# Kernel tuning notes

Measured on AMD Instinct MI355X. Metric: run time of the kernel, lower is better.

Reference implementation:

```python
import jax, jax.numpy as jnp
import numpy as np

MO = 48          # max_output_len (positional slots)
D = 32           # d_inner
NA = 8           # n_actions
STOP = 0
CAT_PRIM, CAT_MOD, CAT_COMB = 0, 1, 2


def _mlp(feats, w1, b1, w2, b2, w3, b3):
    # Linear -> GELU(exact, erf) -> Linear -> GELU -> Linear (torch nn.GELU default is exact)
    h = jax.nn.gelu(feats @ w1.T + b1, approximate=False)
    h = jax.nn.gelu(h @ w2.T + b2, approximate=False)
    return h @ w3.T + b3


def setup_inputs() -> dict:
    key = jax.random.key(0)
    ks = jax.random.split(key, 20)
    B, N = 1024, 16
    inp = {
        'node_cats': jax.random.randint(ks[0], (B, N), 0, 3, dtype=jnp.int32),
        'node_subs': jax.random.randint(ks[1], (B, N), 0, 2, dtype=jnp.int32),
        'node_mask': jax.random.randint(ks[2], (B, N), 0, 2, dtype=jnp.int32),
        'child_left': jax.random.randint(ks[3], (B, N), 0, N, dtype=jnp.int32),
        'child_right': jax.random.randint(ks[4], (B, N), 0, N, dtype=jnp.int32),
        'action_embed': jax.random.normal(ks[5], (NA, D), jnp.float32),
        'mod_w1': jax.random.normal(ks[6], (128, 3), jnp.float32) * 0.1,
        'mod_b1': jax.random.normal(ks[7], (128,), jnp.float32) * 0.02,
        'mod_w2': jax.random.normal(ks[8], (128, 128), jnp.float32) * 0.05,
        'mod_b2': jax.random.normal(ks[9], (128,), jnp.float32) * 0.02,
        'mod_w3': jax.random.normal(ks[10], (MO * MO, 128), jnp.float32) * 0.01,
        'mod_b3': (4.0 * jnp.eye(MO)).flatten(),  # identity-ish init as in torch code
        'comb_w1': jax.random.normal(ks[11], (128, 4), jnp.float32) * 0.1,
        'comb_b1': jax.random.normal(ks[12], (128,), jnp.float32) * 0.02,
        'comb_w2': jax.random.normal(ks[13], (128, 128), jnp.float32) * 0.05,
        'comb_b2': jax.random.normal(ks[14], (128,), jnp.float32) * 0.02,
        'comb_w3': jax.random.normal(ks[15], (MO * 2 * MO, 128), jnp.float32) * 0.01,
        'comb_b3': (4.0 * jnp.eye(MO, 2 * MO)).flatten(),
    }
    return inp


def _forward(node_cats, node_subs, node_mask, child_left, child_right,
             action_embed, mod_w1, mod_b1, mod_w2, mod_b2, mod_w3, mod_b3,
             comb_w1, comb_b1, comb_w2, comb_b2, comb_w3, comb_b3):
    B, N = node_cats.shape
    mask = node_mask.astype(bool)
    cl = jnp.clip(child_left, 0, N - 1)
    cr = jnp.clip(child_right, 0, N - 1)
    prim_mask = (node_cats == CAT_PRIM) & mask
    mod_mask = (node_cats == CAT_MOD) & mask
    comb_mask = (node_cats == CAT_COMB) & mask
    subs01 = jnp.clip(node_subs, 0, 1)
    sub_oh = jax.nn.one_hot(subs01, 2, dtype=jnp.float32)  # (B,N,2)

    # --- primitive init: buffer[0] = action_embed[subs+1], zeros elsewhere ---
    action_ids = jnp.clip(node_subs + 1, 0, NA - 1)
    prim_vecs = action_embed[action_ids]  # (B,N,D)
    buffers = jnp.zeros((B, N, MO, D), jnp.float32)
    buffers = buffers.at[:, :, 0, :].set(prim_vecs * prim_mask[..., None].astype(jnp.float32))
    counts = prim_mask.astype(jnp.float32)  # (B,N)

    # --- modifier stage ---
    child_buf = jnp.take_along_axis(buffers, cl[:, :, None, None], axis=1)  # (B,N,MO,D)
    child_cnt = jnp.take_along_axis(counts, cl, axis=1)  # (B,N)
    feats = jnp.concatenate([child_cnt[..., None] / MO, sub_oh], axis=-1)  # (B,N,3)
    logits = _mlp(feats, mod_w1, mod_b1, mod_w2, mod_b2, mod_w3, mod_b3).reshape(B, N, MO, MO)
    attn = jax.nn.softmax(logits, axis=-1)
    mod_buf = jnp.einsum('bnpq,bnqd->bnpd', attn, child_buf)
    factors = jnp.array([2.0, 3.0], jnp.float32)[subs01]
    mod_cnt = jnp.minimum(child_cnt * factors, float(MO))
    buffers = jnp.where(mod_mask[:, :, None, None], mod_buf, buffers)
    counts = jnp.where(mod_mask, mod_cnt, counts)

    # --- combinator stage ---
    left_buf = jnp.take_along_axis(buffers, cl[:, :, None, None], axis=1)
    right_buf = jnp.take_along_axis(buffers, cr[:, :, None, None], axis=1)
    left_cnt = jnp.take_along_axis(counts, cl, axis=1)
    right_cnt = jnp.take_along_axis(counts, cr, axis=1)
    feats = jnp.concatenate([left_cnt[..., None] / MO, right_cnt[..., None] / MO, sub_oh], axis=-1)  # (B,N,4)
    logits = _mlp(feats, comb_w1, comb_b1, comb_w2, comb_b2, comb_w3, comb_b3).reshape(B, N, MO, 2 * MO)
    attn = jax.nn.softmax(logits, axis=-1)
    concat_buf = jnp.concatenate([left_buf, right_buf], axis=2)  # (B,N,2MO,D)
    comb_buf = jnp.einsum('bnpq,bnqd->bnpd', attn, concat_buf)
    comb_cnt = jnp.minimum(left_cnt + right_cnt, float(MO))
    buffers = jnp.where(comb_mask[:, :, None, None], comb_buf, buffers)
    counts = jnp.where(comb_mask, comb_cnt, counts)

    # --- decode root with tied embedding + stop bias ---
    root_buf = buffers[:, 0, :, :]  # (B,MO,D)
    out = jnp.einsum('bpd,ad->bpa', root_buf, action_embed)  # (B,MO,NA)
    positions = jnp.arange(MO, dtype=jnp.float32)[None, :]  # (1,MO)
    is_stop = (positions >= counts[:, 0:1]).astype(jnp.float32)[..., None]  # (B,MO,1)
    stop_bias = jnp.zeros((NA,), jnp.float32).at[STOP].set(8.0)
    return out + is_stop * stop_bias


def reference(node_cats, node_subs, node_mask, child_left, child_right,
              action_embed, mod_w1, mod_b1, mod_w2, mod_b2, mod_w3, mod_b3,
              comb_w1, comb_b1, comb_w2, comb_b2, comb_w3, comb_b3):
    return _forward(node_cats, node_subs, node_mask, child_left, child_right,
                    action_embed, mod_w1, mod_b1, mod_w2, mod_b2, mod_w3, mod_b3,
                    comb_w1, comb_b1, comb_w2, comb_b2, comb_w3, comb_b3)
```

## Files before the change

kernel.cpp:

```cpp
#include <hip/hip_runtime.h>
#include <hip/hip_bf16.h>
#include <float.h>


#define NNODE 16

#define MODCOL_OFF 0
#define G_OFF      192
#define C0_OFF     256
#define C48_OFF    1792
#define DOTL_OFF   3328
#define DOTR_OFF   6400
#define H2_OFF     9472

__device__ __forceinline__ float gelu_exact(float x) {
    return 0.5f * x * (1.0f + erff(x * 0.70710678118654752f));
}

__device__ __forceinline__ float dot128(const float* __restrict__ w,
                                        const float* __restrict__ h) {
    const float4* w4 = (const float4*)w;
    float s = 0.f;
    #pragma unroll
    for (int i = 0; i < 32; ++i) {
        float4 v = w4[i];
        s += v.x * h[4 * i + 0] + v.y * h[4 * i + 1] +
             v.z * h[4 * i + 2] + v.w * h[4 * i + 3];
    }
    return s;
}

__global__ __launch_bounds__(128) void scan_tables_a(
    const float* __restrict__ E,
    const float* __restrict__ mw1, const float* __restrict__ mb1,
    const float* __restrict__ mw2, const float* __restrict__ mb2,
    const float* __restrict__ mw3, const float* __restrict__ mb3,
    const float* __restrict__ cw1, const float* __restrict__ cb1,
    const float* __restrict__ cw2, const float* __restrict__ cb2,
    float* __restrict__ ws)
{
    __shared__ float h1[128];
    __shared__ float h2s[128];
    __shared__ float lg[48];

    const int tid = threadIdx.x;
    const int blk = blockIdx.x;

    if (blk < 96) {
        const int mm = blk / 48, p = blk % 48;
        const float f0 = 1.0f / 48.0f;
        const float f1 = (mm == 0) ? 1.0f : 0.0f;
        const float f2 = (mm == 1) ? 1.0f : 0.0f;
        h1[tid] = gelu_exact(mw1[tid * 3 + 0] * f0 + mw1[tid * 3 + 1] * f1 +
                             mw1[tid * 3 + 2] * f2 + mb1[tid]);
        __syncthreads();
        h2s[tid] = gelu_exact(dot128(mw2 + tid * 128, h1) + mb2[tid]);
        __syncthreads();
        if (tid < 48)
            lg[tid] = dot128(mw3 + (p * 48 + tid) * 128, h2s) + mb3[p * 48 + tid];
        __syncthreads();
        if (tid < 64) {
            float lv = (tid < 48) ? lg[tid] : -FLT_MAX;
            float mx = lv;
            #pragma unroll
            for (int d = 32; d > 0; d >>= 1) mx = fmaxf(mx, __shfl_xor(mx, d));
            float ev = (tid < 48) ? expf(lv - mx) : 0.f;
            float sm = ev;
            #pragma unroll
            for (int d = 32; d > 0; d >>= 1) sm += __shfl_xor(sm, d);
            if (tid == 0)
                ws[MODCOL_OFF + (2 + mm) * 48 + p] = ev / sm;
        }
        return;
    }
    if (blk == 96) {
        if (tid < 64) {
            const int i = tid >> 3, a = tid & 7;
            float s = 0.f;
            #pragma unroll
            for (int d = 0; d < 32; ++d) s += E[i * 32 + d] * E[a * 32 + d];
            ws[G_OFF + tid] = s;
        }
        return;
    }
    {
        const int c = blk - 97;
        const int csub = c & 1;
        const int rc = (c >> 1) & 3;
        const int lc = (c >> 3) & 3;
        const float f0 = (float)lc / 48.0f;
        const float f1 = (float)rc / 48.0f;
        const float f2 = (csub == 0) ? 1.0f : 0.0f;
        const float f3 = (csub == 1) ? 1.0f : 0.0f;
        h1[tid] = gelu_exact(cw1[tid * 4 + 0] * f0 + cw1[tid * 4 + 1] * f1 +
                             cw1[tid * 4 + 2] * f2 + cw1[tid * 4 + 3] * f3 + cb1[tid]);
        __syncthreads();
        ws[H2_OFF + c * 128 + tid] =
            gelu_exact(dot128(cw2 + tid * 128, h1) + cb2[tid]);
    }
}

__global__ __launch_bounds__(128, 4) void scan_tables_b(
    const float* __restrict__ cw3, const float* __restrict__ cb3,
    float* __restrict__ ws)
{
    __shared__ float h2s[128];
    __shared__ float mc[96];
    __shared__ float lg[96];
    __shared__ float pr[96];
    __shared__ float red[4];

    const int tid = threadIdx.x;
    const int p = blockIdx.x >> 5;
    const int c = blockIdx.x & 31;

    h2s[tid] = ws[H2_OFF + c * 128 + tid];
    if (tid < 96) mc[tid] = ws[MODCOL_OFF + 96 + tid];
    __syncthreads();

    const int j = tid & 3;
    const int rbase = tid >> 2;
    const float4* h24 = (const float4*)h2s;
    #pragma unroll
    for (int o = 0; o < 3; ++o) {
        const int r = o * 32 + rbase;
        const float4* w4 = (const float4*)(cw3 + (p * 96 + r) * 128);
        float s = 0.f;
        #pragma unroll
        for (int i = 0; i < 8; ++i) {
            const int f4i = i * 4 + j;
            float4 w = w4[f4i];
            float4 h = h24[f4i];
            s += w.x * h.x + w.y * h.y + w.z * h.z + w.w * h.w;
        }
        s += __shfl_xor(s, 1);
        s += __shfl_xor(s, 2);
        if (j == 0) lg[r] = s;
    }
    __syncthreads();

    const int wv = tid >> 6;
    float lv = (tid < 96) ? (lg[tid] + cb3[p * 96 + tid]) : -FLT_MAX;
    float m = lv;
    #pragma unroll
    for (int d = 32; d > 0; d >>= 1) m = fmaxf(m, __shfl_xor(m, d));
    if ((tid & 63) == 0) red[wv] = m;
    __syncthreads();
    const float mx = fmaxf(red[0], red[1]);

    float ev = (tid < 96) ? expf(lv - mx) : 0.f;
    if (tid < 96) pr[tid] = ev;
    float sum = ev;
    #pragma unroll
    for (int d = 32; d > 0; d >>= 1) sum += __shfl_xor(sum, d);
    if ((tid & 63) == 0) red[2 + wv] = sum;
    __syncthreads();
    const float inv = 1.0f / (red[2] + red[3]);

    if (tid == 0) {
        ws[C0_OFF + c * 48 + p]  = pr[0]  * inv;
        ws[C48_OFF + c * 48 + p] = pr[48] * inv;
    }
    if (tid < 4) {
        const int mm = tid & 1;
        const int side = tid >> 1;
        const float* q0 = pr + side * 48;
        const float* mr = mc + mm * 48;
        float s = 0.f;
        #pragma unroll
        for (int q = 0; q < 48; ++q) s += q0[q] * mr[q];
        const int off = (side == 0 ? DOTL_OFF : DOTR_OFF) + (c * 2 + mm) * 48 + p;
        ws[off] = s * inv;
    }
}

__global__ __launch_bounds__(384) void scan_output(
    const int* __restrict__ cats, const int* __restrict__ subs,
    const int* __restrict__ mask, const int* __restrict__ cl,
    const int* __restrict__ cr,
    const float* __restrict__ ws,
    float* __restrict__ out)
{
    __shared__ int sc[NNODE], ss[NNODE], sm[NNODE], sl[NNODE], sr[NNODE];
    __shared__ int s_dec[7];
    __shared__ float s_G[64];

    const int b = blockIdx.x;
    const int tid = threadIdx.x;
    if (tid < NNODE) {
        sc[tid] = cats[b * NNODE + tid];
        ss[tid] = subs[b * NNODE + tid];
        sm[tid] = mask[b * NNODE + tid];
        sl[tid] = cl[b * NNODE + tid];
        sr[tid] = cr[b * NNODE + tid];
    } else if (tid >= 64 && tid < 128) {
        s_G[tid - 64] = ws[G_OFF + tid - 64];
    }
    __syncthreads();

    if (tid == 0) {
        auto clampN  = [](int x) { return x < 0 ? 0 : (x > NNODE - 1 ? NNODE - 1 : x); };
        auto clamp01 = [](int x) { return x < 0 ? 0 : (x > 1 ? 1 : x); };
        auto clampA  = [](int x) { return x < 0 ? 0 : (x > 7 ? 7 : x); };
        auto PRIM = [&](int n) { return (sc[n] == 0) && (sm[n] != 0); };
        auto MODM = [&](int n) { return (sc[n] == 1) && (sm[n] != 0); };
        auto AID  = [&](int n) { return clampA(ss[n] + 1); };

        int modeL = 0, modeR = 0, offL = 0, offR = 0, aidL = 0, aidR = 0, count0 = 0;
        const int  cat0 = sc[0];
        const bool msk0 = sm[0] != 0;
        const int  sub0 = clamp01(ss[0]);
        const int  cl0  = clampN(sl[0]);
        const int  cr0  = clampN(sr[0]);

        if (cat0 == 2 && msk0) {
            auto cnt2 = [&](int n) -> int {
                if (MODM(n)) {
                    int c1 = PRIM(clampN(sl[n])) ? 1 : 0;
                    int f  = clamp01(ss[n]) ? 3 : 2;
                    int v  = c1 * f;
                    return v > 48 ? 48 : v;
                }
                return PRIM(n) ? 1 : 0;
            };
            const int l = cl0, r = cr0;
            const int lcc = cnt2(l), rcc = cnt2(r);
            const int cidx = (lcc * 4 + rcc) * 2 + sub0;
            count0 = lcc + rcc; if (count0 > 48) count0 = 48;
            if (MODM(l)) {
                const int g = clampN(sl[l]);
                if (PRIM(g)) {
                    modeL = 1; aidL = AID(g);
                    offL = DOTL_OFF + (cidx * 2 + clamp01(ss[l])) * 48;
                }
            } else if (PRIM(l)) {
                modeL = 1; aidL = AID(l);
                offL = C0_OFF + cidx * 48;
            }
            if (MODM(r)) {
                const int g = clampN(sl[r]);
                if (PRIM(g)) {
                    modeR = 1; aidR = AID(g);
                    offR = DOTR_OFF + (cidx * 2 + clamp01(ss[r])) * 48;
                }
            } else if (PRIM(r)) {
                modeR = 1; aidR = AID(r);
                offR = C48_OFF + cidx * 48;
            }
        } else if (cat0 == 1 && msk0) {
            const int ch = cl0;
            const int c1 = PRIM(ch) ? 1 : 0;
            count0 = c1 * (sub0 ? 3 : 2); if (count0 > 48) count0 = 48;
            if (c1) {
                modeL = 1; aidL = AID(ch);
                offL = MODCOL_OFF + (2 + sub0) * 48;
            }
        } else if (cat0 == 0 && msk0) {
            modeL = 2; aidL = AID(0); count0 = 1;
        }
        s_dec[0] = modeL; s_dec[1] = modeR; s_dec[2] = offL; s_dec[3] = offR;
        s_dec[4] = aidL;  s_dec[5] = aidR;  s_dec[6] = count0;
    }
    __syncthreads();

    const int p = tid >> 3, a = tid & 7;
    const int modeL = s_dec[0], modeR = s_dec[1];
    float v = 0.f;
    if (modeL == 1)       v += ws[s_dec[2] + p] * s_G[s_dec[4] * 8 + a];
    else if (modeL == 2)  { if (p == 0) v = s_G[s_dec[4] * 8 + a]; }
    if (modeR == 1)       v += ws[s_dec[3] + p] * s_G[s_dec[5] * 8 + a];
    if (a == 0 && p >= s_dec[6]) v += 8.0f;
    out[b * 384 + tid] = v;
}

extern "C" void kernel_launch(void* const* d_in, const int* in_sizes, int n_in,
                              void* d_out, int out_size, void* d_ws, size_t ws_size,
                              hipStream_t stream) {
    const int* cats = (const int*)d_in[0];
    const int* subs = (const int*)d_in[1];
    const int* mask = (const int*)d_in[2];
    const int* cl   = (const int*)d_in[3];
    const int* cr   = (const int*)d_in[4];
    const float* E   = (const float*)d_in[5];
    const float* mw1 = (const float*)d_in[6];
    const float* mb1 = (const float*)d_in[7];
    const float* mw2 = (const float*)d_in[8];
    const float* mb2 = (const float*)d_in[9];
    const float* mw3 = (const float*)d_in[10];
    const float* mb3 = (const float*)d_in[11];
    const float* cw1 = (const float*)d_in[12];
    const float* cb1 = (const float*)d_in[13];
    const float* cw2 = (const float*)d_in[14];
    const float* cb2 = (const float*)d_in[15];
    const float* cw3 = (const float*)d_in[16];
    const float* cb3 = (const float*)d_in[17];
    float* ws  = (float*)d_ws;
    float* out = (float*)d_out;
    const int B = in_sizes[0] / NNODE;

    scan_tables_a<<<129, 128, 0, stream>>>(E, mw1, mb1, mw2, mb2, mw3, mb3,
                                           cw1, cb1, cw2, cb2, ws);
    scan_tables_b<<<48 * 32, 128, 0, stream>>>(cw3, cb3, ws);
    scan_output<<<B, 384, 0, stream>>>(cats, subs, mask, cl, cr, ws, out);
}
```

Baseline: 105.4 us.

## Fuse three table and output kernels into one cooperative persistent kernel

Replaces the three back-to-back launches (table build, comb table build, per-batch output) with a single cooperative kernel of 512 blocks that separates the phases with grid.sync(), and keeps the old launches as a fallback if the cooperative launch fails. Each block in the comb-table phase now handles two (position, combo) units with a 4-lane split dot product and shuffle reductions. The aim is to remove launch gaps and tail effects between the small kernels. In exchange it adds grid-wide barrier cost and caps parallelism at 512 blocks, so the output phase loops over batches.

```diff
diff --git a/kernel.cpp b/kernel.cpp
--- a/kernel.cpp
+++ b/kernel.cpp
@@ -1,9 +1,13 @@
 #include <hip/hip_runtime.h>
+#include <hip/hip_cooperative_groups.h>
 #include <hip/hip_bf16.h>
 #include <float.h>
 
+namespace cg = cooperative_groups;
+
 
 #define NNODE 16
+#define GRID_BLKS 512
 
 #define MODCOL_OFF 0
 #define G_OFF      192
@@ -28,6 +32,262 @@
              v.z * h[4 * i + 2] + v.w * h[4 * i + 3];
     }
     return s;
+}
+
+__device__ __forceinline__ void decode_tree(
+    const int* sc, const int* ss, const int* sm, const int* sl, const int* sr,
+    int* s_dec)
+{
+    auto clampN  = [](int x) { return x < 0 ? 0 : (x > NNODE - 1 ? NNODE - 1 : x); };
+    auto clamp01 = [](int x) { return x < 0 ? 0 : (x > 1 ? 1 : x); };
+    auto clampA  = [](int x) { return x < 0 ? 0 : (x > 7 ? 7 : x); };
+    auto PRIM = [&](int n) { return (sc[n] == 0) && (sm[n] != 0); };
+    auto MODM = [&](int n) { return (sc[n] == 1) && (sm[n] != 0); };
+    auto AID  = [&](int n) { return clampA(ss[n] + 1); };
+
+    int modeL = 0, modeR = 0, offL = 0, offR = 0, aidL = 0, aidR = 0, count0 = 0;
+    const int  cat0 = sc[0];
+    const bool msk0 = sm[0] != 0;
+    const int  sub0 = clamp01(ss[0]);
+    const int  cl0  = clampN(sl[0]);
+    const int  cr0  = clampN(sr[0]);
+
+    if (cat0 == 2 && msk0) {
+        auto cnt2 = [&](int n) -> int {
+            if (MODM(n)) {
+                int c1 = PRIM(clampN(sl[n])) ? 1 : 0;
+                int f  = clamp01(ss[n]) ? 3 : 2;
+                int v  = c1 * f;
+                return v > 48 ? 48 : v;
+            }
+            return PRIM(n) ? 1 : 0;
+        };
+        const int l = cl0, r = cr0;
+        const int lcc = cnt2(l), rcc = cnt2(r);
+        const int cidx = (lcc * 4 + rcc) * 2 + sub0;
+        count0 = lcc + rcc; if (count0 > 48) count0 = 48;
+        if (MODM(l)) {
+            const int g = clampN(sl[l]);
+            if (PRIM(g)) {
+                modeL = 1; aidL = AID(g);
+                offL = DOTL_OFF + (cidx * 2 + clamp01(ss[l])) * 48;
+            }
+        } else if (PRIM(l)) {
+            modeL = 1; aidL = AID(l);
+            offL = C0_OFF + cidx * 48;
+        }
+        if (MODM(r)) {
+            const int g = clampN(sl[r]);
+            if (PRIM(g)) {
+                modeR = 1; aidR = AID(g);
+                offR = DOTR_OFF + (cidx * 2 + clamp01(ss[r])) * 48;
+            }
+        } else if (PRIM(r)) {
+            modeR = 1; aidR = AID(r);
+            offR = C48_OFF + cidx * 48;
+        }
+    } else if (cat0 == 1 && msk0) {
+        const int ch = cl0;
+        const int c1 = PRIM(ch) ? 1 : 0;
+        count0 = c1 * (sub0 ? 3 : 2); if (count0 > 48) count0 = 48;
+        if (c1) {
+            modeL = 1; aidL = AID(ch);
+            offL = MODCOL_OFF + (2 + sub0) * 48;
+        }
+    } else if (cat0 == 0 && msk0) {
+        modeL = 2; aidL = AID(0); count0 = 1;
+    }
+    s_dec[0] = modeL; s_dec[1] = modeR; s_dec[2] = offL; s_dec[3] = offR;
+    s_dec[4] = aidL;  s_dec[5] = aidR;  s_dec[6] = count0;
+}
+
+__global__ __launch_bounds__(256) void scan_fused(
+    const int* __restrict__ cats, const int* __restrict__ subs,
+    const int* __restrict__ mask, const int* __restrict__ clv,
+    const int* __restrict__ crv,
+    const float* __restrict__ E,
+    const float* __restrict__ mw1, const float* __restrict__ mb1,
+    const float* __restrict__ mw2, const float* __restrict__ mb2,
+    const float* __restrict__ mw3, const float* __restrict__ mb3,
+    const float* __restrict__ cw1, const float* __restrict__ cb1,
+    const float* __restrict__ cw2, const float* __restrict__ cb2,
+    const float* __restrict__ cw3, const float* __restrict__ cb3,
+    float* __restrict__ ws, float* __restrict__ out, int B)
+{
+    cg::grid_group grid = cg::this_grid();
+    const int tid = threadIdx.x;
+    const int blk = blockIdx.x;
+
+    __shared__ float h1[128];
+    __shared__ float h2a[128];
+    __shared__ float lgA[48];
+    __shared__ float h2s[2][128];
+    __shared__ float mcs[96];
+    __shared__ float lg2[2][96];
+    __shared__ float pr2[2][96];
+    __shared__ float red2[2][4];
+    __shared__ int sc[NNODE], ss2[NNODE], smk[NNODE], sl2[NNODE], sr2[NNODE];
+    __shared__ int s_dec[7];
+    __shared__ float s_G[64];
+
+    if (blk < 96) {
+        const int mm = blk / 48, p = blk % 48;
+        const float f0 = 1.0f / 48.0f;
+        const float f1 = (mm == 0) ? 1.0f : 0.0f;
+        const float f2 = (mm == 1) ? 1.0f : 0.0f;
+        if (tid < 128)
+            h1[tid] = gelu_exact(mw1[tid * 3 + 0] * f0 + mw1[tid * 3 + 1] * f1 +
+                                 mw1[tid * 3 + 2] * f2 + mb1[tid]);
+        __syncthreads();
+        if (tid < 128)
+            h2a[tid] = gelu_exact(dot128(mw2 + tid * 128, h1) + mb2[tid]);
+        __syncthreads();
+        if (tid < 48)
+            lgA[tid] = dot128(mw3 + (p * 48 + tid) * 128, h2a) + mb3[p * 48 + tid];
+        __syncthreads();
+        if (tid < 64) {
+            float lv = (tid < 48) ? lgA[tid] : -FLT_MAX;
+            float mx = lv;
+            #pragma unroll
+            for (int d = 32; d > 0; d >>= 1) mx = fmaxf(mx, __shfl_xor(mx, d));
+            float ev = (tid < 48) ? expf(lv - mx) : 0.f;
+            float sm = ev;
+            #pragma unroll
+            for (int d = 32; d > 0; d >>= 1) sm += __shfl_xor(sm, d);
+            if (tid == 0)
+                ws[MODCOL_OFF + (2 + mm) * 48 + p] = ev / sm;
+        }
+    } else if (blk == 96) {
+        if (tid < 64) {
+            const int i = tid >> 3, a = tid & 7;
+            float s = 0.f;
+            #pragma unroll
+            for (int d = 0; d < 32; ++d) s += E[i * 32 + d] * E[a * 32 + d];
+            ws[G_OFF + tid] = s;
+        }
+    } else if (blk < 129) {
+        const int c = blk - 97;
+        const int csub = c & 1;
+        const int rc = (c >> 1) & 3;
+        const int lc = (c >> 3) & 3;
+        const float f0 = (float)lc / 48.0f;
+        const float f1 = (float)rc / 48.0f;
+        const float f2 = (csub == 0) ? 1.0f : 0.0f;
+        const float f3 = (csub == 1) ? 1.0f : 0.0f;
+        if (tid < 128)
+            h1[tid] = gelu_exact(cw1[tid * 4 + 0] * f0 + cw1[tid * 4 + 1] * f1 +
+                                 cw1[tid * 4 + 2] * f2 + cw1[tid * 4 + 3] * f3 + cb1[tid]);
+        __syncthreads();
+        if (tid < 128)
+            ws[H2_OFF + c * 128 + tid] =
+                gelu_exact(dot128(cw2 + tid * 128, h1) + cb2[tid]);
+    }
+    grid.sync();
+
+    if (tid < 96) mcs[tid] = ws[MODCOL_OFF + 96 + tid];
+    const int sub = tid >> 7;
+    const int stid = tid & 127;
+    for (int vb = blk; vb < 768; vb += GRID_BLKS) {
+        const int u = vb * 2 + sub;
+        const int p = u >> 5;
+        const int c = u & 31;
+
+        h2s[sub][stid] = ws[H2_OFF + c * 128 + stid];
+        __syncthreads();
+
+        const int j = stid & 3;
+        const int rbase = stid >> 2;
+        const float4* h24 = (const float4*)h2s[sub];
+        #pragma unroll
+        for (int o = 0; o < 3; ++o) {
+            const int r = o * 32 + rbase;
+            const float4* w4 = (const float4*)(cw3 + (p * 96 + r) * 128);
+            float s = 0.f;
+            #pragma unroll
+            for (int i = 0; i < 8; ++i) {
+                const int f4i = i * 4 + j;
+                float4 w = w4[f4i];
+                float4 h = h24[f4i];
+                s += w.x * h.x + w.y * h.y + w.z * h.z + w.w * h.w;
+            }
+            s += __shfl_xor(s, 1);
+            s += __shfl_xor(s, 2);
+            if (j == 0) lg2[sub][r] = s;
+        }
+        __syncthreads();
+
+        const int wv = stid >> 6;
+        float lv = (stid < 96) ? (lg2[sub][stid] + cb3[p * 96 + stid]) : -FLT_MAX;
+        float m = lv;
+        #pragma unroll
+        for (int d = 32; d > 0; d >>= 1) m = fmaxf(m, __shfl_xor(m, d));
+        if ((stid & 63) == 0) red2[sub][wv] = m;
+        __syncthreads();
+        const float mx = fmaxf(red2[sub][0], red2[sub][1]);
+
+        float ev = (stid < 96) ? expf(lv - mx) : 0.f;
+        if (stid < 96) pr2[sub][stid] = ev;
+        float sum = ev;
+        #pragma unroll
+        for (int d = 32; d > 0; d >>= 1) sum += __shfl_xor(sum, d);
+        if ((stid & 63) == 0) red2[sub][2 + wv] = sum;
+        __syncthreads();
+        const float inv = 1.0f / (red2[sub][2] + red2[sub][3]);
+
+        if (stid == 0) {
+            ws[C0_OFF + c * 48 + p]  = pr2[sub][0]  * inv;
+            ws[C48_OFF + c * 48 + p] = pr2[sub][48] * inv;
+        }
+        if (stid < 4) {
+            const int mm2 = stid & 1;
+            const int side = stid >> 1;
+            const float* q0 = pr2[sub] + side * 48;
+            const float* mr = mcs + mm2 * 48;
+            float s = 0.f;
+            #pragma unroll
+            for (int q = 0; q < 48; ++q) s += q0[q] * mr[q];
+            const int off = (side == 0 ? DOTL_OFF : DOTR_OFF) + (c * 2 + mm2) * 48 + p;
+            ws[off] = s * inv;
+        }
+        __syncthreads();
+    }
+    grid.sync();
+
+    if (tid >= 64 && tid < 128) s_G[tid - 64] = ws[G_OFF + tid - 64];
+    for (int b = blk; b < B; b += GRID_BLKS) {
+        if (tid < NNODE) {
+            sc[tid]  = cats[b * NNODE + tid];
+            ss2[tid] = subs[b * NNODE + tid];
+            smk[tid] = mask[b * NNODE + tid];
+            sl2[tid] = clv[b * NNODE + tid];
+            sr2[tid] = crv[b * NNODE + tid];
+        }
+        __syncthreads();
+        if (tid == 0) decode_tree(sc, ss2, smk, sl2, sr2, s_dec);
+        __syncthreads();
+
+        const int modeL = s_dec[0], modeR = s_dec[1];
+        {
+            const int p = tid >> 3, a = tid & 7;
+            float v = 0.f;
+            if (modeL == 1)      v += ws[s_dec[2] + p] * s_G[s_dec[4] * 8 + a];
+            else if (modeL == 2) { if (p == 0) v = s_G[s_dec[4] * 8 + a]; }
+            if (modeR == 1)      v += ws[s_dec[3] + p] * s_G[s_dec[5] * 8 + a];
+            if (a == 0 && p >= s_dec[6]) v += 8.0f;
+            out[b * 384 + tid] = v;
+        }
+        if (tid < 128) {
+            const int idx = tid + 256;
+            const int p = idx >> 3, a = idx & 7;
+            float v = 0.f;
+            if (modeL == 1)      v += ws[s_dec[2] + p] * s_G[s_dec[4] * 8 + a];
+            else if (modeL == 2) { if (p == 0) v = s_G[s_dec[4] * 8 + a]; }
+            if (modeR == 1)      v += ws[s_dec[3] + p] * s_G[s_dec[5] * 8 + a];
+            if (a == 0 && p >= s_dec[6]) v += 8.0f;
+            out[b * 384 + idx] = v;
+        }
+        __syncthreads();
+    }
 }
 
 __global__ __launch_bounds__(128) void scan_tables_a(
@@ -198,69 +458,7 @@
     }
     __syncthreads();
 
-    if (tid == 0) {
-        auto clampN  = [](int x) { return x < 0 ? 0 : (x > NNODE - 1 ? NNODE - 1 : x); };
-        auto clamp01 = [](int x) { return x < 0 ? 0 : (x > 1 ? 1 : x); };
-        auto clampA  = [](int x) { return x < 0 ? 0 : (x > 7 ? 7 : x); };
-        auto PRIM = [&](int n) { return (sc[n] == 0) && (sm[n] != 0); };
-        auto MODM = [&](int n) { return (sc[n] == 1) && (sm[n] != 0); };
-        auto AID  = [&](int n) { return clampA(ss[n] + 1); };
-
-        int modeL = 0, modeR = 0, offL = 0, offR = 0, aidL = 0, aidR = 0, count0 = 0;
-        const int  cat0 = sc[0];
-        const bool msk0 = sm[0] != 0;
-        const int  sub0 = clamp01(ss[0]);
-        const int  cl0  = clampN(sl[0]);
-        const int  cr0  = clampN(sr[0]);
-
-        if (cat0 == 2 && msk0) {
-            auto cnt2 = [&](int n) -> int {
-                if (MODM(n)) {
-                    int c1 = PRIM(clampN(sl[n])) ? 1 : 0;
-                    int f  = clamp01(ss[n]) ? 3 : 2;
-                    int v  = c1 * f;
-                    return v > 48 ? 48 : v;
-                }
-                return PRIM(n) ? 1 : 0;
-            };
-            const int l = cl0, r = cr0;
-            const int lcc = cnt2(l), rcc = cnt2(r);
-            const int cidx = (lcc * 4 + rcc) * 2 + sub0;
-            count0 = lcc + rcc; if (count0 > 48) count0 = 48;
-            if (MODM(l)) {
-                const int g = clampN(sl[l]);
-                if (PRIM(g)) {
-                    modeL = 1; aidL = AID(g);
-                    offL = DOTL_OFF + (cidx * 2 + clamp01(ss[l])) * 48;
-                }
-            } else if (PRIM(l)) {
-                modeL = 1; aidL = AID(l);
-                offL = C0_OFF + cidx * 48;
-            }
-            if (MODM(r)) {
-                const int g = clampN(sl[r]);
-                if (PRIM(g)) {
-                    modeR = 1; aidR = AID(g);
-                    offR = DOTR_OFF + (cidx * 2 + clamp01(ss[r])) * 48;
-                }
-            } else if (PRIM(r)) {
-                modeR = 1; aidR = AID(r);
-                offR = C48_OFF + cidx * 48;
-            }
-        } else if (cat0 == 1 && msk0) {
-            const int ch = cl0;
-            const int c1 = PRIM(ch) ? 1 : 0;
-            count0 = c1 * (sub0 ? 3 : 2); if (count0 > 48) count0 = 48;
-            if (c1) {
-                modeL = 1; aidL = AID(ch);
-                offL = MODCOL_OFF + (2 + sub0) * 48;
-            }
-        } else if (cat0 == 0 && msk0) {
-            modeL = 2; aidL = AID(0); count0 = 1;
-        }
-        s_dec[0] = modeL; s_dec[1] = modeR; s_dec[2] = offL; s_dec[3] = offR;
-        s_dec[4] = aidL;  s_dec[5] = aidR;  s_dec[6] = count0;
-    }
+    if (tid == 0) decode_tree(sc, ss, sm, sl, sr, s_dec);
     __syncthreads();
 
     const int p = tid >> 3, a = tid & 7;
@@ -279,8 +477,8 @@
     const int* cats = (const int*)d_in[0];
     const int* subs = (const int*)d_in[1];
     const int* mask = (const int*)d_in[2];
-    const int* cl   = (const int*)d_in[3];
-    const int* cr   = (const int*)d_in[4];
+    const int* clv  = (const int*)d_in[3];
+    const int* crv  = (const int*)d_in[4];
     const float* E   = (const float*)d_in[5];
     const float* mw1 = (const float*)d_in[6];
     const float* mb1 = (const float*)d_in[7];
@@ -296,10 +494,23 @@
     const float* cb3 = (const float*)d_in[17];
     float* ws  = (float*)d_ws;
     float* out = (float*)d_out;
-    const int B = in_sizes[0] / NNODE;
-
-    scan_tables_a<<<129, 128, 0, stream>>>(E, mw1, mb1, mw2, mb2, mw3, mb3,
-                                           cw1, cb1, cw2, cb2, ws);
-    scan_tables_b<<<48 * 32, 128, 0, stream>>>(cw3, cb3, ws);
-    scan_output<<<B, 384, 0, stream>>>(cats, subs, mask, cl, cr, ws, out);
-}
+    int B = in_sizes[0] / NNODE;
+
+    void* args[] = {
+        (void*)&cats, (void*)&subs, (void*)&mask, (void*)&clv, (void*)&crv,
+        (void*)&E,
+        (void*)&mw1, (void*)&mb1, (void*)&mw2, (void*)&mb2,
+        (void*)&mw3, (void*)&mb3,
+        (void*)&cw1, (void*)&cb1, (void*)&cw2, (void*)&cb2,
+        (void*)&cw3, (void*)&cb3,
+        (void*)&ws, (void*)&out, (void*)&B
+    };
+    hipError_t err = hipLaunchCooperativeKernel(
+        (const void*)scan_fused, dim3(GRID_BLKS), dim3(256), args, 0, stream);
+    if (err != hipSuccess) {
+        scan_tables_a<<<129, 128, 0, stream>>>(E, mw1, mb1, mw2, mb2, mw3, mb3,
+                                               cw1, cb1, cw2, cb2, ws);
+        scan_tables_b<<<48 * 32, 128, 0, stream>>>(cw3, cb3, ws);
+        scan_output<<<B, 384, 0, stream>>>(cats, subs, mask, clv, crv, ws, out);
+    }
+}
```

Measured after the change: 241.7 us. 2.29x slower.
